# Optimization experiments

Hardware: AMD Instinct MI355X
Metric: run time of the kernel (lower is better)

Reference implementation:

```python
import jax, jax.numpy as jnp
import numpy as np


def _gru_scan(x_seq, Wih, Whh, bih, bhh):
    # x_seq: (S, N, D); PyTorch GRU/GRUCell gate math, h0 = 0. Returns (S, N, H).
    H = Whh.shape[1]
    gi_all = x_seq @ Wih.T + bih  # precompute input projections: (S, N, 3H)

    def step(h, gi):
        gh = h @ Whh.T + bhh
        ir, iz, inn = jnp.split(gi, 3, axis=-1)
        hr, hz, hn = jnp.split(gh, 3, axis=-1)
        r = jax.nn.sigmoid(ir + hr)
        z = jax.nn.sigmoid(iz + hz)
        n = jnp.tanh(inn + r * hn)
        h_new = (1.0 - z) * n + z * h
        return h_new, h_new

    h0 = jnp.zeros((x_seq.shape[1], H), x_seq.dtype)
    _, ys = jax.lax.scan(step, h0, gi_all)
    return ys


def setup_inputs() -> dict:
    key = jax.random.key(0)
    ks = jax.random.split(key, 40)
    B, T = 32, 800
    NOTE, E, P, H0, H1, FE, RE = 128, 256, 256, 512, 512, 64, 64

    def w(k, shape):
        return jax.random.normal(k, shape, dtype=jnp.float32) * 0.05

    return {
        "note": jax.random.randint(ks[0], (B, T), 0, NOTE, dtype=jnp.int64),
        "f0_prev": jax.random.normal(ks[1], (B, T), dtype=jnp.float32),
        "rmse_prev": jax.random.normal(ks[2], (B, T), dtype=jnp.float32),
        "note_emb": w(ks[3], (NOTE, E)),
        "f0_W": w(ks[4], (FE, 1)), "f0_b": w(ks[5], (FE,)),
        "rmse_W": w(ks[6], (RE, 1)), "rmse_b": w(ks[7], (RE,)),
        "pre1_W": w(ks[8], (P, E)), "pre1_b": w(ks[9], (P,)),
        "pre2_W": w(ks[10], (P, P)), "pre2_b": w(ks[11], (P,)),
        "encf_Wih": w(ks[12], (3 * H0, P)), "encf_Whh": w(ks[13], (3 * H0, H0)),
        "encf_bih": w(ks[14], (3 * H0,)), "encf_bhh": w(ks[15], (3 * H0,)),
        "encb_Wih": w(ks[16], (3 * H0, P)), "encb_Whh": w(ks[17], (3 * H0, H0)),
        "encb_bih": w(ks[18], (3 * H0,)), "encb_bhh": w(ks[19], (3 * H0,)),
        "decf_Wih": w(ks[20], (3 * H1, 2 * H0 + FE)), "decf_Whh": w(ks[21], (3 * H1, H1)),
        "decf_bih": w(ks[22], (3 * H1,)), "decf_bhh": w(ks[23], (3 * H1,)),
        "decr_Wih": w(ks[24], (3 * H1, 2 * H0 + RE)), "decr_Whh": w(ks[25], (3 * H1, H1)),
        "decr_bih": w(ks[26], (3 * H1,)), "decr_bhh": w(ks[27], (3 * H1,)),
        "postf_W": w(ks[28], (1, H1)), "postf_b": w(ks[29], (1,)),
        "postr_W": w(ks[30], (1, H1)), "postr_b": w(ks[31], (1,)),
    }


def reference(note, f0_prev, rmse_prev, note_emb, f0_W, f0_b, rmse_W, rmse_b,
              pre1_W, pre1_b, pre2_W, pre2_b,
              encf_Wih, encf_Whh, encf_bih, encf_bhh,
              encb_Wih, encb_Whh, encb_bih, encb_bhh,
              decf_Wih, decf_Whh, decf_bih, decf_bhh,
              decr_Wih, decr_Whh, decr_bih, decr_bhh,
              postf_W, postf_b, postr_W, postr_b):
    # Embeddings. Linear(1, FE) on a [B,T] signal == outer-broadcast with W[:,0].
    ne = note_emb[note]                                   # (B, T, E)
    f0e = f0_prev[..., None] * f0_W[:, 0] + f0_b          # (B, T, FE)
    rme = rmse_prev[..., None] * rmse_W[:, 0] + rmse_b    # (B, T, RE)

    # Prenet: Linear -> Tanh -> Linear -> Tanh
    h = jnp.tanh(jnp.tanh(ne @ pre1_W.T + pre1_b) @ pre2_W.T + pre2_b)  # (B, T, P)

    # Encoder: torch nn.GRU built WITHOUT batch_first and called with lengths=None,
    # so the recurrence runs over axis 0 (B) with T acting as the GRU batch. Replicated.
    ef = _gru_scan(h, encf_Wih, encf_Whh, encf_bih, encf_bhh)            # (B, T, H0)
    eb = _gru_scan(h[::-1], encb_Wih, encb_Whh, encb_bih, encb_bhh)[::-1]
    enc = jnp.concatenate([ef, eb], axis=-1)                             # (B, T, 2H0)

    # Decoders: GRUCell loop over T with teacher forcing (y_prevs has T>1 steps),
    # so step-t input is concat(enc[:, t], embed(prev[:, t])) -> standard scan.
    xt = jnp.transpose(enc, (1, 0, 2))                                   # (T, B, 2H0)
    hf = _gru_scan(jnp.concatenate([xt, jnp.transpose(f0e, (1, 0, 2))], -1),
                   decf_Wih, decf_Whh, decf_bih, decf_bhh)               # (T, B, H1)
    hr = _gru_scan(jnp.concatenate([xt, jnp.transpose(rme, (1, 0, 2))], -1),
                   decr_Wih, decr_Whh, decr_bih, decr_bhh)               # (T, B, H1)

    f0 = jnp.transpose((hf @ postf_W.T + postf_b)[..., 0], (1, 0))       # (B, T)
    rmse = jnp.transpose((hr @ postr_W.T + postr_b)[..., 0], (1, 0))     # (B, T)
    return (f0, rmse)
```

## Files before the change

kernel.cpp:

```cpp
#include <hip/hip_runtime.h>
#include <hip/hip_bf16.h>


typedef __bf16 bf16;
typedef bf16 bf16x8 __attribute__((ext_vector_type(8)));
typedef float f32x4 __attribute__((ext_vector_type(4)));
typedef unsigned int u32x4 __attribute__((ext_vector_type(4)));

#define BATCH 32
#define TLEN 800
#define BT (BATCH * TLEN)

__device__ __forceinline__ float bf2f(bf16 v) {
    unsigned short u = __builtin_bit_cast(unsigned short, v);
    unsigned int x = ((unsigned int)u) << 16;
    return __builtin_bit_cast(float, x);
}
__device__ __forceinline__ bf16 f2bf(float f) {
    unsigned int x = __builtin_bit_cast(unsigned int, f);
    unsigned int r = (x + 0x7FFFu + ((x >> 16) & 1u)) >> 16;
    return __builtin_bit_cast(bf16, (unsigned short)r);
}
__device__ __forceinline__ bf16x8 ld8f(const float* p) {
    f32x4 a = *(const f32x4*)p;
    f32x4 b = *(const f32x4*)(p + 4);
    bf16x8 r;
#pragma unroll
    for (int i = 0; i < 4; i++) {
        r[i] = f2bf(a[i]);
        r[i + 4] = f2bf(b[i]);
    }
    return r;
}
__device__ __forceinline__ void splitv(f32x4 a, f32x4 b, bf16x8& vh, bf16x8& vl) {
#pragma unroll
    for (int j = 0; j < 4; j++) {
        bf16 h0 = f2bf(a[j]);
        vh[j] = h0;
        vl[j] = f2bf(a[j] - bf2f(h0));
        bf16 h1 = f2bf(b[j]);
        vh[j + 4] = h1;
        vl[j + 4] = f2bf(b[j] - bf2f(h1));
    }
}
__device__ __forceinline__ f32x4 mfma16(bf16x8 a, bf16x8 b, f32x4 c) {
    return __builtin_amdgcn_mfma_f32_16x16x32_bf16(a, b, c, 0, 0, 0);
}
__device__ __forceinline__ float sigm(float x) { return 1.f / (1.f + __expf(-x)); }

__device__ __forceinline__ void cst_u32(unsigned int* p, unsigned int v) {
    __hip_atomic_store(p, v, __ATOMIC_RELAXED, __HIP_MEMORY_SCOPE_AGENT);
}
__device__ __forceinline__ unsigned int cld_u32(const unsigned int* p) {
    return __hip_atomic_load(p, __ATOMIC_RELAXED, __HIP_MEMORY_SCOPE_AGENT);
}
__device__ __forceinline__ unsigned long long cld_u64(const unsigned int* p) {
    return __hip_atomic_load((const unsigned long long*)p, __ATOMIC_RELAXED,
                             __HIP_MEMORY_SCOPE_AGENT);
}
__device__ __forceinline__ float pk2f(unsigned int pk) {
    return bf2f(__builtin_bit_cast(bf16, (unsigned short)(pk >> 16))) +
           bf2f(__builtin_bit_cast(bf16, (unsigned short)(pk & 0xFFFFu)));
}
__device__ __forceinline__ void unpk(const unsigned long long q[4], bf16x8& ah,
                                     bf16x8& al) {
    u32x4 hw, lw;
#pragma unroll
    for (int i = 0; i < 4; i++) {
        unsigned int x = (unsigned int)q[i];
        unsigned int y = (unsigned int)(q[i] >> 32);
        hw[i] = __builtin_amdgcn_perm(y, x, 0x07060302u);
        lw[i] = __builtin_amdgcn_perm(y, x, 0x05040100u);
    }
    ah = __builtin_bit_cast(bf16x8, hw);
    al = __builtin_bit_cast(bf16x8, lw);
}

template <int MODE>
__global__ __launch_bounds__(256) void gemm01_k(
    const int* __restrict__ note, const float* __restrict__ asrc,
    const float* __restrict__ W, const float* __restrict__ bias,
    float* __restrict__ out, int t0, int TC) {
    __shared__ bf16 Ah[128][72], Al[128][72], Bs[128][72];

    const int tid = threadIdx.x;
    const int lane = tid & 63, wv = tid >> 6;
    const int wm = wv & 1, wn = wv >> 1;
    const int l15 = lane & 15, hi = lane >> 4;
    const int bm = blockIdx.x * 128, bn = blockIdx.y * 128;
    const int ch = (tid & 7) * 8, arow = tid >> 3;

    f32x4 acc[4][4] = {};
    const float* ap[4];
    if (MODE == 0) {
        int zc = 0;
        for (int i = 0; i < 64; i++) zc += (note[2 * i + 1] == 0) ? 1 : 0;
        const bool n64 = (zc >= 60);
#pragma unroll
        for (int i = 0; i < 4; i++) {
            int m = bm + arow + 32 * i;
            int b = m / TC, tt = m - b * TC;
            int idx = b * TLEN + t0 + tt;
            int id = n64 ? note[2 * idx] : note[idx];
            id = id < 0 ? 0 : (id > 127 ? 127 : id);
            ap[i] = asrc + (size_t)id * 256;
        }
    } else {
#pragma unroll
        for (int i = 0; i < 4; i++) ap[i] = asrc + (size_t)(bm + arow + 32 * i) * 256;
    }

    for (int k0 = 0; k0 < 256; k0 += 64) {
#pragma unroll
        for (int i = 0; i < 4; i++) {
            int row = arow + 32 * i;
            f32x4 va = *(const f32x4*)(ap[i] + k0 + ch);
            f32x4 vb = *(const f32x4*)(ap[i] + k0 + ch + 4);
            bf16x8 vh, vl;
            splitv(va, vb, vh, vl);
            *(bf16x8*)&Ah[row][ch] = vh;
            *(bf16x8*)&Al[row][ch] = vl;
        }
#pragma unroll
        for (int i = 0; i < 4; i++) {
            int row = arow + 32 * i;
            *(bf16x8*)&Bs[row][ch] = ld8f(W + (size_t)(bn + row) * 256 + k0 + ch);
        }
        __syncthreads();
#pragma unroll
        for (int kk = 0; kk < 64; kk += 32) {
            bf16x8 ah[4], al[4], bb[4];
#pragma unroll
            for (int mt = 0; mt < 4; mt++) {
                ah[mt] = *(const bf16x8*)&Ah[wm * 64 + mt * 16 + l15][kk + hi * 8];
                al[mt] = *(const bf16x8*)&Al[wm * 64 + mt * 16 + l15][kk + hi * 8];
            }
#pragma unroll
            for (int nt = 0; nt < 4; nt++)
                bb[nt] = *(const bf16x8*)&Bs[wn * 64 + nt * 16 + l15][kk + hi * 8];
#pragma unroll
            for (int mt = 0; mt < 4; mt++)
#pragma unroll
                for (int nt = 0; nt < 4; nt++) {
                    acc[mt][nt] = mfma16(ah[mt], bb[nt], acc[mt][nt]);
                    acc[mt][nt] = mfma16(al[mt], bb[nt], acc[mt][nt]);
                }
        }
        __syncthreads();
    }

#pragma unroll
    for (int mt = 0; mt < 4; mt++)
#pragma unroll
        for (int nt = 0; nt < 4; nt++) {
            int n = bn + wn * 64 + nt * 16 + l15;
            float bs = bias[n];
#pragma unroll
            for (int r = 0; r < 4; r++) {
                int m = bm + wm * 64 + mt * 16 + hi * 4 + r;
                out[(size_t)m * 256 + n] = tanhf(acc[mt][nt][r] + bs);
            }
        }
}

__global__ __launch_bounds__(256) void gemm2_k(
    const float* __restrict__ ef, const float* __restrict__ eb,
    const float* __restrict__ sig, const float* __restrict__ sigW,
    const float* __restrict__ sigB, const float* __restrict__ W,
    const float* __restrict__ bias, float* __restrict__ out, int t0, int TC) {
    __shared__ bf16 Ah[128][72], Al[128][72];
    __shared__ bf16 Bh[64][72], Bl[64][72];

    const int tid = threadIdx.x;
    const int lane = tid & 63, wv = tid >> 6;
    const int wm = wv & 1, wn = wv >> 1;
    const int l15 = lane & 15, hi = lane >> 4;
    const int bm = blockIdx.x * 128, bn = blockIdx.y * 64;
    const int ch = (tid & 7) * 8, arow = tid >> 3;

    f32x4 acc[4][2] = {};
    int rb[4];
    float sigv[4];
#pragma unroll
    for (int i = 0; i < 4; i++) {
        int m = bm + arow + 32 * i;
        int tt = m >> 5, b = m & 31;
        rb[i] = b * TC + tt;
        sigv[i] = sig[b * TLEN + t0 + tt];
    }

    for (int k0 = 0; k0 < 1088; k0 += 64) {
#pragma unroll
        for (int i = 0; i < 4; i++) {
            int row = arow + 32 * i;
            int k = k0 + ch;
            f32x4 va, vb;
            if (k < 512) {
                va = *(const f32x4*)(ef + (size_t)rb[i] * 512 + k);
                vb = *(const f32x4*)(ef + (size_t)rb[i] * 512 + k + 4);
            } else if (k < 1024) {
                va = *(const f32x4*)(eb + (size_t)rb[i] * 512 + (k - 512));
                vb = *(const f32x4*)(eb + (size_t)rb[i] * 512 + (k - 512) + 4);
            } else {
                f32x4 w0 = *(const f32x4*)(sigW + ch);
                f32x4 w1 = *(const f32x4*)(sigW + ch + 4);
                f32x4 b0 = *(const f32x4*)(sigB + ch);
                f32x4 b1 = *(const f32x4*)(sigB + ch + 4);
                float s = sigv[i];
#pragma unroll
                for (int j = 0; j < 4; j++) {
                    va[j] = s * w0[j] + b0[j];
                    vb[j] = s * w1[j] + b1[j];
                }
            }
            bf16x8 vh, vl;
            splitv(va, vb, vh, vl);
            *(bf16x8*)&Ah[row][ch] = vh;
            *(bf16x8*)&Al[row][ch] = vl;
        }
#pragma unroll
        for (int i = 0; i < 2; i++) {
            int row = arow + 32 * i;
            const float* src = W + (size_t)(bn + row) * 1088 + k0 + ch;
            f32x4 va = *(const f32x4*)src;
            f32x4 vb = *(const f32x4*)(src + 4);
            bf16x8 vh, vl;
            splitv(va, vb, vh, vl);
            *(bf16x8*)&Bh[row][ch] = vh;
            *(bf16x8*)&Bl[row][ch] = vl;
        }
        __syncthreads();
#pragma unroll
        for (int kk = 0; kk < 64; kk += 32) {
            bf16x8 ah[4], al[4], bh[2], bl[2];
#pragma unroll
            for (int mt = 0; mt < 4; mt++) {
                ah[mt] = *(const bf16x8*)&Ah[wm * 64 + mt * 16 + l15][kk + hi * 8];
                al[mt] = *(const bf16x8*)&Al[wm * 64 + mt * 16 + l15][kk + hi * 8];
            }
#pragma unroll
            for (int nt = 0; nt < 2; nt++) {
                bh[nt] = *(const bf16x8*)&Bh[wn * 32 + nt * 16 + l15][kk + hi * 8];
                bl[nt] = *(const bf16x8*)&Bl[wn * 32 + nt * 16 + l15][kk + hi * 8];
            }
#pragma unroll
            for (int mt = 0; mt < 4; mt++)
#pragma unroll
                for (int nt = 0; nt < 2; nt++) {
                    acc[mt][nt] = mfma16(ah[mt], bh[nt], acc[mt][nt]);
                    acc[mt][nt] = mfma16(al[mt], bh[nt], acc[mt][nt]);
                    acc[mt][nt] = mfma16(ah[mt], bl[nt], acc[mt][nt]);
                }
        }
        __syncthreads();
    }

#pragma unroll
    for (int mt = 0; mt < 4; mt++)
#pragma unroll
        for (int nt = 0; nt < 2; nt++) {
            int n = bn + wn * 32 + nt * 16 + l15;
            float bs = bias[n];
#pragma unroll
            for (int r = 0; r < 4; r++) {
                int m = bm + wm * 64 + mt * 16 + hi * 4 + r;
                out[(size_t)m * 1536 + n] = acc[mt][nt][r] + bs;
            }
        }
}

__global__ __launch_bounds__(256) void enc_step_k(
    int step, int TC, const float* __restrict__ hpre, float* __restrict__ efb,
    float* __restrict__ ebb, const float* __restrict__ fWih,
    const float* __restrict__ fWhh, const float* __restrict__ fbih,
    const float* __restrict__ fbhh, const float* __restrict__ bWih,
    const float* __restrict__ bWhh, const float* __restrict__ bbih,
    const float* __restrict__ bbhh) {
    __shared__ bf16 As[32][72], Alo[32][72];
    __shared__ bf16 Bs[96][72], Blo[96][72];

    const int dir = blockIdx.z;
    const float* Wih = dir ? bWih : fWih;
    const float* Whh = dir ? bWhh : fWhh;
    const float* bih = dir ? bbih : fbih;
    const float* bhh = dir ? bbhh : fbhh;
    float* outb = dir ? ebb : efb;
    const int bsrc = dir ? (31 - step) : step;
    const int prevb = dir ? (32 - step) : (step - 1);

    const int tid = threadIdx.x;
    const int lane = tid & 63, wv = tid >> 6;
    const int mt = wv & 1, jt = wv >> 1;
    const int l15 = lane & 15, hi = lane >> 4;
    const int mtile = blockIdx.x, jtile = blockIdx.y;
    const int ch = (tid & 7) * 8, arow = tid >> 3;

    f32x4 acc_r = {}, acc_z = {}, acc_in = {}, acc_hn = {};

    const int nblocks = (step == 0) ? 4 : 12;
    for (int kb = 0; kb < nblocks; kb++) {
        int k0 = kb * 64;
        {
            int trow = mtile * 32 + arow;
            int tcl = trow < TC ? trow : TC - 1;
            const float* src = (k0 < 256)
                                   ? (hpre + ((size_t)bsrc * TC + tcl) * 256 + k0 + ch)
                                   : (outb + ((size_t)prevb * TC + tcl) * 512 + (k0 - 256) + ch);
            f32x4 va = *(const f32x4*)src;
            f32x4 vb = *(const f32x4*)(src + 4);
            bf16x8 vh, vl;
            splitv(va, vb, vh, vl);
            *(bf16x8*)&As[arow][ch] = vh;
            *(bf16x8*)&Alo[arow][ch] = vl;
        }
#pragma unroll
        for (int i = 0; i < 3; i++) {
            int row = arow + 32 * i;
            int s = row >> 5, j = row & 31;
            int wr = s * 512 + jtile * 32 + j;
            const float* src = (k0 < 256) ? (Wih + (size_t)wr * 256 + k0 + ch)
                                          : (Whh + (size_t)wr * 512 + (k0 - 256) + ch);
            f32x4 va = *(const f32x4*)src;
            f32x4 vb = *(const f32x4*)(src + 4);
            bf16x8 vh, vl;
            splitv(va, vb, vh, vl);
            *(bf16x8*)&Bs[row][ch] = vh;
            *(bf16x8*)&Blo[row][ch] = vl;
        }
        __syncthreads();
#pragma unroll
        for (int kk = 0; kk < 64; kk += 32) {
            bf16x8 a = *(const bf16x8*)&As[mt * 16 + l15][kk + hi * 8];
            bf16x8 alo = *(const bf16x8*)&Alo[mt * 16 + l15][kk + hi * 8];
            bf16x8 brh = *(const bf16x8*)&Bs[jt * 16 + l15][kk + hi * 8];
            bf16x8 brl = *(const bf16x8*)&Blo[jt * 16 + l15][kk + hi * 8];
            bf16x8 bzh = *(const bf16x8*)&Bs[32 + jt * 16 + l15][kk + hi * 8];
            bf16x8 bzl = *(const bf16x8*)&Blo[32 + jt * 16 + l15][kk + hi * 8];
            bf16x8 bnh = *(const bf16x8*)&Bs[64 + jt * 16 + l15][kk + hi * 8];
            bf16x8 bnl = *(const bf16x8*)&Blo[64 + jt * 16 + l15][kk + hi * 8];
            acc_r = mfma16(a, brh, acc_r);
            acc_r = mfma16(alo, brh, acc_r);
            acc_r = mfma16(a, brl, acc_r);
            acc_z = mfma16(a, bzh, acc_z);
            acc_z = mfma16(alo, bzh, acc_z);
            acc_z = mfma16(a, bzl, acc_z);
            if (k0 < 256) {
                acc_in = mfma16(a, bnh, acc_in);
                acc_in = mfma16(alo, bnh, acc_in);
                acc_in = mfma16(a, bnl, acc_in);
            } else {
                acc_hn = mfma16(a, bnh, acc_hn);
                acc_hn = mfma16(alo, bnh, acc_hn);
                acc_hn = mfma16(a, bnl, acc_hn);
            }
        }
        __syncthreads();
    }

    int j = jtile * 32 + jt * 16 + l15;
    float bir = bih[j] + bhh[j];
    float biz = bih[512 + j] + bhh[512 + j];
    float bin = bih[1024 + j];
    float bhn = bhh[1024 + j];
#pragma unroll
    for (int r = 0; r < 4; r++) {
        int trow = mtile * 32 + mt * 16 + hi * 4 + r;
        if (trow < TC) {
            float rr = sigm(acc_r[r] + bir);
            float zz = sigm(acc_z[r] + biz);
            float nn = tanhf(acc_in[r] + bin + rr * (acc_hn[r] + bhn));
            float hp = (step > 0) ? outb[((size_t)prevb * TC + trow) * 512 + j] : 0.f;
            outb[((size_t)bsrc * TC + trow) * 512 + j] = (1.f - zz) * nn + zz * hp;
        }
    }
}

__global__ __launch_bounds__(256, 1) void dec_k(
    const float* __restrict__ giF, const float* __restrict__ giR,
    const float* __restrict__ WhhF, const float* __restrict__ WhhR,
    const float* __restrict__ bhhF, const float* __restrict__ bhhR,
    unsigned int* __restrict__ HpkF, unsigned int* __restrict__ HpkR,
    const unsigned int* __restrict__ HpvF, const unsigned int* __restrict__ HpvR,
    int* __restrict__ flags, int t0, int TC) {
    const int d = blockIdx.x >> 4;
    const int g = blockIdx.x & 15;
    const float* gi = d ? giR : giF;
    const float* Whh = d ? WhhR : WhhF;
    const float* bhh = d ? bhhR : bhhF;
    unsigned int* Hpk = d ? HpkR : HpkF;
    const unsigned int* Hpv = d ? HpvR : HpvF;
    int* flg = flags + d * 256;

    const int tid = threadIdx.x;
    const int lane = tid & 63, wv = tid >> 6;
    const int mt = wv & 1, jt = wv >> 1;
    const int l15 = lane & 15, hi = lane >> 4;
    const int j_abs = g * 32 + jt * 16 + l15;
    const int wid = g * 4 + wv;

    bf16x8 Wf[3][16];
#pragma unroll
    for (int s = 0; s < 3; s++)
#pragma unroll
        for (int kb = 0; kb < 16; kb++)
            Wf[s][kb] = ld8f(Whh + (size_t)(s * 512 + j_abs) * 512 + kb * 32 + hi * 8);

    const float bhr = bhh[j_abs];
    const float bhz = bhh[512 + j_abs];
    const float bhn = bhh[1024 + j_abs];

    float hpreg[4] = {0.f, 0.f, 0.f, 0.f};

    for (int tt = 0; tt < TC; tt++) {
        const int t = t0 + tt;
        float gr[4], gz[4], gn[4];
#pragma unroll
        for (int r = 0; r < 4; r++) {
            int b = mt * 16 + hi * 4 + r;
            const float* gp = gi + ((size_t)tt * BATCH + b) * 1536 + j_abs;
            gr[r] = gp[0];
            gz[r] = gp[512];
            gn[r] = gp[1024];
        }

        f32x4 ar = {}, az = {}, an = {};
        float hp[4] = {0.f, 0.f, 0.f, 0.f};
        if (t > 0) {
            const unsigned int* base;
            if (tt > 0) {
                while (true) {
                    int v = __hip_atomic_load(&flg[lane * 4], __ATOMIC_RELAXED,
                                              __HIP_MEMORY_SCOPE_AGENT);
                    if (!__any(v < t)) break;
                    __builtin_amdgcn_s_sleep(1);
                }
                asm volatile("" ::: "memory");
                base = Hpk + (size_t)(tt - 1) * BATCH * 512;
            } else {
                base = Hpv + (size_t)(TC - 1) * BATCH * 512;
            }
            const unsigned int* ap = base + (size_t)(mt * 16 + l15) * 512 + hi * 8;
#pragma unroll
            for (int half = 0; half < 2; half++) {
                unsigned long long q[8][4];
#pragma unroll
                for (int qq = 0; qq < 8; qq++) {
                    const unsigned int* pp = ap + (half * 8 + qq) * 32;
#pragma unroll
                    for (int u = 0; u < 4; u++) q[qq][u] = cld_u64(pp + 2 * u);
                }
#pragma unroll
                for (int qq = 0; qq < 8; qq++) {
                    int kb = half * 8 + qq;
                    bf16x8 ah, al;
                    unpk(q[qq], ah, al);
                    ar = mfma16(ah, Wf[0][kb], ar);
                    ar = mfma16(al, Wf[0][kb], ar);
                    az = mfma16(ah, Wf[1][kb], az);
                    az = mfma16(al, Wf[1][kb], az);
                    an = mfma16(ah, Wf[2][kb], an);
                    an = mfma16(al, Wf[2][kb], an);
                }
            }
            if (tt > 0) {
#pragma unroll
                for (int r = 0; r < 4; r++) hp[r] = hpreg[r];
            } else {
#pragma unroll
                for (int r = 0; r < 4; r++) {
                    int b = mt * 16 + hi * 4 + r;
                    hp[r] = pk2f(cld_u32(base + (size_t)b * 512 + j_abs));
                }
            }
        }
#pragma unroll
        for (int r = 0; r < 4; r++) {
            int b = mt * 16 + hi * 4 + r;
            float rr = sigm(gr[r] + ar[r] + bhr);
            float zz = sigm(gz[r] + az[r] + bhz);
            float nn = tanhf(gn[r] + rr * (an[r] + bhn));
            float hnew = (1.f - zz) * nn + zz * hp[r];
            bf16 hh = f2bf(hnew);
            bf16 hl = f2bf(hnew - bf2f(hh));
            unsigned int pk =
                ((unsigned int)__builtin_bit_cast(unsigned short, hh) << 16) |
                (unsigned int)__builtin_bit_cast(unsigned short, hl);
            cst_u32(&Hpk[((size_t)tt * BATCH + b) * 512 + j_abs], pk);
            hpreg[r] = hnew;
        }
        asm volatile("s_waitcnt vmcnt(0)" ::: "memory");
        if (lane == 0)
            __hip_atomic_store(&flg[wid * 4], t + 1, __ATOMIC_RELAXED,
                               __HIP_MEMORY_SCOPE_AGENT);
    }
}

__global__ __launch_bounds__(256) void post_k(
    const unsigned int* __restrict__ H, const float* __restrict__ W,
    const float* __restrict__ bs, float* __restrict__ out, int t0) {
    const int wv = threadIdx.x >> 6, lane = threadIdx.x & 63;
    const int row = blockIdx.x * 4 + wv;
    const int tt = row >> 5, b = row & 31;
    const float bias = bs[0];
    const unsigned int* hp = H + (size_t)row * 512 + lane * 8;
    u32x4 p0 = *(const u32x4*)hp;
    u32x4 p1 = *(const u32x4*)(hp + 4);
    f32x4 w0 = *(const f32x4*)(W + lane * 8);
    f32x4 w1 = *(const f32x4*)(W + lane * 8 + 4);
    float s = 0.f;
#pragma unroll
    for (int i = 0; i < 4; i++) s += pk2f(p0[i]) * w0[i] + pk2f(p1[i]) * w1[i];
#pragma unroll
    for (int off = 32; off > 0; off >>= 1) s += __shfl_down(s, off);
    if (lane == 0) out[b * TLEN + t0 + tt] = s + bias;
}

__global__ void zero_k(int* __restrict__ flags) {
    int i = blockIdx.x * 256 + threadIdx.x;
    if (i < 2 * TLEN)
        __hip_atomic_store(&flags[i], 0, __ATOMIC_RELAXED,
                           __HIP_MEMORY_SCOPE_AGENT);
}

extern "C" void kernel_launch(void* const* d_in, const int* in_sizes, int n_in,
                              void* d_out, int out_size, void* d_ws, size_t ws_size,
                              hipStream_t stream) {
    const int* note = (const int*)d_in[0];
    const float* f0_prev = (const float*)d_in[1];
    const float* rmse_prev = (const float*)d_in[2];
    const float* note_emb = (const float*)d_in[3];
    const float* f0_W = (const float*)d_in[4];
    const float* f0_b = (const float*)d_in[5];
    const float* rmse_W = (const float*)d_in[6];
    const float* rmse_b = (const float*)d_in[7];
    const float* pre1_W = (const float*)d_in[8];
    const float* pre1_b = (const float*)d_in[9];
    const float* pre2_W = (const float*)d_in[10];
    const float* pre2_b = (const float*)d_in[11];
    const float* encf_Wih = (const float*)d_in[12];
    const float* encf_Whh = (const float*)d_in[13];
    const float* encf_bih = (const float*)d_in[14];
    const float* encf_bhh = (const float*)d_in[15];
    const float* encb_Wih = (const float*)d_in[16];
    const float* encb_Whh = (const float*)d_in[17];
    const float* encb_bih = (const float*)d_in[18];
    const float* encb_bhh = (const float*)d_in[19];
    const float* decf_Wih = (const float*)d_in[20];
    const float* decf_Whh = (const float*)d_in[21];
    const float* decf_bih = (const float*)d_in[22];
    const float* decf_bhh = (const float*)d_in[23];
    const float* decr_Wih = (const float*)d_in[24];
    const float* decr_Whh = (const float*)d_in[25];
    const float* decr_bih = (const float*)d_in[26];
    const float* decr_bhh = (const float*)d_in[27];
    const float* postf_W = (const float*)d_in[28];
    const float* postf_b = (const float*)d_in[29];
    const float* postr_W = (const float*)d_in[30];
    const float* postr_b = (const float*)d_in[31];
    float* out = (float*)d_out;

    const int tcs[9] = {800, 400, 200, 100, 80, 40, 20, 8, 4};
    int TC = 4;
    for (int i = 0; i < 9; i++) {
        int tc = tcs[i];
        int slots = (tc == TLEN) ? 1 : 2;
        size_t need = (size_t)(2 * 65536 + 2 * 196608 + 2 * slots * 65536) * tc + 65536;
        if (ws_size >= need) { TC = tc; break; }
    }
    const int NC = TLEN / TC;
    const int slots = (NC == 1) ? 1 : 2;

    char* ws = (char*)d_ws;
    size_t off = 0;
    auto carve = [&](size_t bytes) {
        void* p = ws + off;
        off += (bytes + 255) & ~(size_t)255;
        return p;
    };
    const size_t slotB = (size_t)65536 * TC;
    float* ef_c = (float*)carve(slotB);
    float* eb_c = (float*)carve(slotB);
    float* giF_c = (float*)carve((size_t)196608 * TC);
    float* giR_c = (float*)carve((size_t)196608 * TC);
    unsigned int* ringF = (unsigned int*)carve(slotB * slots);
    unsigned int* ringR = (unsigned int*)carve(slotB * slots);
    int* flags = (int*)carve(2 * TLEN * 4);
    float* t1_c = giF_c;
    float* hpre_c = giF_c + (size_t)8192 * TC;

    zero_k<<<dim3(7), 256, 0, stream>>>(flags);

    const size_t slotE = (size_t)TC * BATCH * 512;

    for (int c = 0; c < NC; c++) {
        const int t0 = c * TC;
        const int mg = TC * 32 / 128;

        gemm01_k<0><<<dim3(mg, 2), 256, 0, stream>>>(note, note_emb, pre1_W, pre1_b,
                                                     t1_c, t0, TC);
        gemm01_k<1><<<dim3(mg, 2), 256, 0, stream>>>(nullptr, t1_c, pre2_W, pre2_b,
                                                     hpre_c, t0, TC);
        const int etiles = (TC + 31) / 32;
        for (int i = 0; i < 32; i++)
            enc_step_k<<<dim3(etiles, 16, 2), 256, 0, stream>>>(
                i, TC, hpre_c, ef_c, eb_c, encf_Wih, encf_Whh, encf_bih, encf_bhh,
                encb_Wih, encb_Whh, encb_bih, encb_bhh);

        gemm2_k<<<dim3(mg, 24), 256, 0, stream>>>(ef_c, eb_c, f0_prev, f0_W, f0_b,
                                                  decf_Wih, decf_bih, giF_c, t0, TC);
        gemm2_k<<<dim3(mg, 24), 256, 0, stream>>>(ef_c, eb_c, rmse_prev, rmse_W,
                                                  rmse_b, decr_Wih, decr_bih, giR_c,
                                                  t0, TC);

        unsigned int* HcurF = ringF + (size_t)(c & (slots - 1)) * slotE;
        const unsigned int* HprevF = ringF + (size_t)((c - 1) & (slots - 1)) * slotE;
        unsigned int* HcurR = ringR + (size_t)(c & (slots - 1)) * slotE;
        const unsigned int* HprevR = ringR + (size_t)((c - 1) & (slots - 1)) * slotE;

        dec_k<<<dim3(32), 256, 0, stream>>>(giF_c, giR_c, decf_Whh, decr_Whh,
                                            decf_bhh, decr_bhh, HcurF, HcurR,
                                            HprevF, HprevR, flags, t0, TC);

        post_k<<<dim3(TC * 32 / 4), 256, 0, stream>>>(HcurF, postf_W, postf_b,
                                                      out, t0);
        post_k<<<dim3(TC * 32 / 4), 256, 0, stream>>>(HcurR, postr_W, postr_b,
                                                      out + BT, t0);
    }
    (void)in_sizes; (void)n_in; (void)out_size; (void)ws_size;
}
```

Measured before the change: 12.61 ms.

## Hoist encoder input projection into batched GEMM and widen decoder blocks

The encoder input projection (hpre @ Wih) now runs as one batched GEMM per direction (a new MODE 2 of gemm01_k) before the 32 sequential encoder steps. Each step then loads the precomputed gates and only does the recurrent Whh matmul, which removes redundant K work from the serial chain. The persistent decoder kernel now runs 16 blocks of 512 threads instead of 32 of 256, so there are fewer flags to poll and one block-level barrier before each flag store. Scratch buffers are reassigned to the ring slots. This adds memory traffic for the precomputed gates and a __syncthreads per decoder timestep.

```diff
diff --git a/kernel.cpp b/kernel.cpp
--- a/kernel.cpp
+++ b/kernel.cpp
@@ -89,6 +89,7 @@
     const int l15 = lane & 15, hi = lane >> 4;
     const int bm = blockIdx.x * 128, bn = blockIdx.y * 128;
     const int ch = (tid & 7) * 8, arow = tid >> 3;
+    const int LDC = (MODE == 2) ? 1536 : 256;
 
     f32x4 acc[4][4] = {};
     const float* ap[4];
@@ -154,11 +155,12 @@
 #pragma unroll
         for (int nt = 0; nt < 4; nt++) {
             int n = bn + wn * 64 + nt * 16 + l15;
-            float bs = bias[n];
+            float bs = (MODE == 2) ? 0.f : bias[n];
 #pragma unroll
             for (int r = 0; r < 4; r++) {
                 int m = bm + wm * 64 + mt * 16 + hi * 4 + r;
-                out[(size_t)m * 256 + n] = tanhf(acc[mt][nt][r] + bs);
+                float v = acc[mt][nt][r] + bs;
+                out[(size_t)m * LDC + n] = (MODE == 2) ? v : tanhf(v);
             }
         }
 }
@@ -270,17 +272,17 @@
 }
 
 __global__ __launch_bounds__(256) void enc_step_k(
-    int step, int TC, const float* __restrict__ hpre, float* __restrict__ efb,
-    float* __restrict__ ebb, const float* __restrict__ fWih,
-    const float* __restrict__ fWhh, const float* __restrict__ fbih,
-    const float* __restrict__ fbhh, const float* __restrict__ bWih,
+    int step, int TC, const float* __restrict__ egiF,
+    const float* __restrict__ egiB, float* __restrict__ efb,
+    float* __restrict__ ebb, const float* __restrict__ fWhh,
+    const float* __restrict__ fbih, const float* __restrict__ fbhh,
     const float* __restrict__ bWhh, const float* __restrict__ bbih,
     const float* __restrict__ bbhh) {
     __shared__ bf16 As[32][72], Alo[32][72];
     __shared__ bf16 Bs[96][72], Blo[96][72];
 
     const int dir = blockIdx.z;
-    const float* Wih = dir ? bWih : fWih;
+    const float* egi = dir ? egiB : egiF;
     const float* Whh = dir ? bWhh : fWhh;
     const float* bih = dir ? bbih : fbih;
     const float* bhh = dir ? bbhh : fbhh;
@@ -294,70 +296,72 @@
     const int l15 = lane & 15, hi = lane >> 4;
     const int mtile = blockIdx.x, jtile = blockIdx.y;
     const int ch = (tid & 7) * 8, arow = tid >> 3;
-
-    f32x4 acc_r = {}, acc_z = {}, acc_in = {}, acc_hn = {};
-
-    const int nblocks = (step == 0) ? 4 : 12;
-    for (int kb = 0; kb < nblocks; kb++) {
-        int k0 = kb * 64;
-        {
-            int trow = mtile * 32 + arow;
-            int tcl = trow < TC ? trow : TC - 1;
-            const float* src = (k0 < 256)
-                                   ? (hpre + ((size_t)bsrc * TC + tcl) * 256 + k0 + ch)
-                                   : (outb + ((size_t)prevb * TC + tcl) * 512 + (k0 - 256) + ch);
-            f32x4 va = *(const f32x4*)src;
-            f32x4 vb = *(const f32x4*)(src + 4);
-            bf16x8 vh, vl;
-            splitv(va, vb, vh, vl);
-            *(bf16x8*)&As[arow][ch] = vh;
-            *(bf16x8*)&Alo[arow][ch] = vl;
-        }
-#pragma unroll
-        for (int i = 0; i < 3; i++) {
-            int row = arow + 32 * i;
-            int s = row >> 5, j = row & 31;
-            int wr = s * 512 + jtile * 32 + j;
-            const float* src = (k0 < 256) ? (Wih + (size_t)wr * 256 + k0 + ch)
-                                          : (Whh + (size_t)wr * 512 + (k0 - 256) + ch);
-            f32x4 va = *(const f32x4*)src;
-            f32x4 vb = *(const f32x4*)(src + 4);
-            bf16x8 vh, vl;
-            splitv(va, vb, vh, vl);
-            *(bf16x8*)&Bs[row][ch] = vh;
-            *(bf16x8*)&Blo[row][ch] = vl;
-        }
-        __syncthreads();
-#pragma unroll
-        for (int kk = 0; kk < 64; kk += 32) {
-            bf16x8 a = *(const bf16x8*)&As[mt * 16 + l15][kk + hi * 8];
-            bf16x8 alo = *(const bf16x8*)&Alo[mt * 16 + l15][kk + hi * 8];
-            bf16x8 brh = *(const bf16x8*)&Bs[jt * 16 + l15][kk + hi * 8];
-            bf16x8 brl = *(const bf16x8*)&Blo[jt * 16 + l15][kk + hi * 8];
-            bf16x8 bzh = *(const bf16x8*)&Bs[32 + jt * 16 + l15][kk + hi * 8];
-            bf16x8 bzl = *(const bf16x8*)&Blo[32 + jt * 16 + l15][kk + hi * 8];
-            bf16x8 bnh = *(const bf16x8*)&Bs[64 + jt * 16 + l15][kk + hi * 8];
-            bf16x8 bnl = *(const bf16x8*)&Blo[64 + jt * 16 + l15][kk + hi * 8];
-            acc_r = mfma16(a, brh, acc_r);
-            acc_r = mfma16(alo, brh, acc_r);
-            acc_r = mfma16(a, brl, acc_r);
-            acc_z = mfma16(a, bzh, acc_z);
-            acc_z = mfma16(alo, bzh, acc_z);
-            acc_z = mfma16(a, bzl, acc_z);
-            if (k0 < 256) {
-                acc_in = mfma16(a, bnh, acc_in);
-                acc_in = mfma16(alo, bnh, acc_in);
-                acc_in = mfma16(a, bnl, acc_in);
-            } else {
+    const int j = jtile * 32 + jt * 16 + l15;
+
+    f32x4 acc_r, acc_z, acc_in;
+    f32x4 acc_hn = {};
+#pragma unroll
+    for (int r = 0; r < 4; r++) {
+        int trow = mtile * 32 + mt * 16 + hi * 4 + r;
+        int tcl = trow < TC ? trow : TC - 1;
+        const float* ep = egi + ((size_t)bsrc * TC + tcl) * 1536 + j;
+        acc_r[r] = ep[0];
+        acc_z[r] = ep[512];
+        acc_in[r] = ep[1024];
+    }
+
+    if (step > 0) {
+        for (int kb = 0; kb < 8; kb++) {
+            int k0 = kb * 64;
+            {
+                int trow = mtile * 32 + arow;
+                int tcl = trow < TC ? trow : TC - 1;
+                const float* src = outb + ((size_t)prevb * TC + tcl) * 512 + k0 + ch;
+                f32x4 va = *(const f32x4*)src;
+                f32x4 vb = *(const f32x4*)(src + 4);
+                bf16x8 vh, vl;
+                splitv(va, vb, vh, vl);
+                *(bf16x8*)&As[arow][ch] = vh;
+                *(bf16x8*)&Alo[arow][ch] = vl;
+            }
+#pragma unroll
+            for (int i = 0; i < 3; i++) {
+                int row = arow + 32 * i;
+                int s = row >> 5, jj = row & 31;
+                const float* src =
+                    Whh + (size_t)(s * 512 + jtile * 32 + jj) * 512 + k0 + ch;
+                f32x4 va = *(const f32x4*)src;
+                f32x4 vb = *(const f32x4*)(src + 4);
+                bf16x8 vh, vl;
+                splitv(va, vb, vh, vl);
+                *(bf16x8*)&Bs[row][ch] = vh;
+                *(bf16x8*)&Blo[row][ch] = vl;
+            }
+            __syncthreads();
+#pragma unroll
+            for (int kk = 0; kk < 64; kk += 32) {
+                bf16x8 a = *(const bf16x8*)&As[mt * 16 + l15][kk + hi * 8];
+                bf16x8 alo = *(const bf16x8*)&Alo[mt * 16 + l15][kk + hi * 8];
+                bf16x8 brh = *(const bf16x8*)&Bs[jt * 16 + l15][kk + hi * 8];
+                bf16x8 brl = *(const bf16x8*)&Blo[jt * 16 + l15][kk + hi * 8];
+                bf16x8 bzh = *(const bf16x8*)&Bs[32 + jt * 16 + l15][kk + hi * 8];
+                bf16x8 bzl = *(const bf16x8*)&Blo[32 + jt * 16 + l15][kk + hi * 8];
+                bf16x8 bnh = *(const bf16x8*)&Bs[64 + jt * 16 + l15][kk + hi * 8];
+                bf16x8 bnl = *(const bf16x8*)&Blo[64 + jt * 16 + l15][kk + hi * 8];
+                acc_r = mfma16(a, brh, acc_r);
+                acc_r = mfma16(alo, brh, acc_r);
+                acc_r = mfma16(a, brl, acc_r);
+                acc_z = mfma16(a, bzh, acc_z);
+                acc_z = mfma16(alo, bzh, acc_z);
+                acc_z = mfma16(a, bzl, acc_z);
                 acc_hn = mfma16(a, bnh, acc_hn);
                 acc_hn = mfma16(alo, bnh, acc_hn);
                 acc_hn = mfma16(a, bnl, acc_hn);
             }
-        }
-        __syncthreads();
-    }
-
-    int j = jtile * 32 + jt * 16 + l15;
+            __syncthreads();
+        }
+    }
+
     float bir = bih[j] + bhh[j];
     float biz = bih[512 + j] + bhh[512 + j];
     float bin = bih[1024 + j];
@@ -375,28 +379,27 @@
     }
 }
 
-__global__ __launch_bounds__(256, 1) void dec_k(
+__global__ __launch_bounds__(512, 1) void dec_k(
     const float* __restrict__ giF, const float* __restrict__ giR,
     const float* __restrict__ WhhF, const float* __restrict__ WhhR,
     const float* __restrict__ bhhF, const float* __restrict__ bhhR,
     unsigned int* __restrict__ HpkF, unsigned int* __restrict__ HpkR,
     const unsigned int* __restrict__ HpvF, const unsigned int* __restrict__ HpvR,
     int* __restrict__ flags, int t0, int TC) {
-    const int d = blockIdx.x >> 4;
-    const int g = blockIdx.x & 15;
+    const int d = blockIdx.x >> 3;
+    const int g = blockIdx.x & 7;
     const float* gi = d ? giR : giF;
     const float* Whh = d ? WhhR : WhhF;
     const float* bhh = d ? bhhR : bhhF;
     unsigned int* Hpk = d ? HpkR : HpkF;
     const unsigned int* Hpv = d ? HpvR : HpvF;
-    int* flg = flags + d * 256;
+    int* flg = flags + d * 64;
 
     const int tid = threadIdx.x;
     const int lane = tid & 63, wv = tid >> 6;
     const int mt = wv & 1, jt = wv >> 1;
     const int l15 = lane & 15, hi = lane >> 4;
-    const int j_abs = g * 32 + jt * 16 + l15;
-    const int wid = g * 4 + wv;
+    const int j_abs = g * 64 + jt * 16 + l15;
 
     bf16x8 Wf[3][16];
 #pragma unroll
@@ -429,7 +432,7 @@
             const unsigned int* base;
             if (tt > 0) {
                 while (true) {
-                    int v = __hip_atomic_load(&flg[lane * 4], __ATOMIC_RELAXED,
+                    int v = __hip_atomic_load(&flg[(lane & 7) * 4], __ATOMIC_RELAXED,
                                               __HIP_MEMORY_SCOPE_AGENT);
                     if (!__any(v < t)) break;
                     __builtin_amdgcn_s_sleep(1);
@@ -489,8 +492,9 @@
             hpreg[r] = hnew;
         }
         asm volatile("s_waitcnt vmcnt(0)" ::: "memory");
-        if (lane == 0)
-            __hip_atomic_store(&flg[wid * 4], t + 1, __ATOMIC_RELAXED,
+        __syncthreads();
+        if (tid == 0)
+            __hip_atomic_store(&flg[g * 4], t + 1, __ATOMIC_RELAXED,
                                __HIP_MEMORY_SCOPE_AGENT);
     }
 }
@@ -585,8 +589,9 @@
     unsigned int* ringF = (unsigned int*)carve(slotB * slots);
     unsigned int* ringR = (unsigned int*)carve(slotB * slots);
     int* flags = (int*)carve(2 * TLEN * 4);
-    float* t1_c = giF_c;
-    float* hpre_c = giF_c + (size_t)8192 * TC;
+
+    float* egiF = giF_c;
+    float* egiB = giR_c;
 
     zero_k<<<dim3(7), 256, 0, stream>>>(flags);
 
@@ -595,16 +600,25 @@
     for (int c = 0; c < NC; c++) {
         const int t0 = c * TC;
         const int mg = TC * 32 / 128;
+        const int cs = c & (slots - 1), ps = (c - 1) & (slots - 1);
+
+        float* t1_c = (float*)(ringF + (size_t)cs * slotE);
+        float* hpre_c = (float*)(ringR + (size_t)cs * slotE);
 
         gemm01_k<0><<<dim3(mg, 2), 256, 0, stream>>>(note, note_emb, pre1_W, pre1_b,
                                                      t1_c, t0, TC);
         gemm01_k<1><<<dim3(mg, 2), 256, 0, stream>>>(nullptr, t1_c, pre2_W, pre2_b,
                                                      hpre_c, t0, TC);
+        gemm01_k<2><<<dim3(mg, 12), 256, 0, stream>>>(nullptr, hpre_c, encf_Wih,
+                                                      nullptr, egiF, t0, TC);
+        gemm01_k<2><<<dim3(mg, 12), 256, 0, stream>>>(nullptr, hpre_c, encb_Wih,
+                                                      nullptr, egiB, t0, TC);
+
         const int etiles = (TC + 31) / 32;
         for (int i = 0; i < 32; i++)
             enc_step_k<<<dim3(etiles, 16, 2), 256, 0, stream>>>(
-                i, TC, hpre_c, ef_c, eb_c, encf_Wih, encf_Whh, encf_bih, encf_bhh,
-                encb_Wih, encb_Whh, encb_bih, encb_bhh);
+                i, TC, egiF, egiB, ef_c, eb_c, encf_Whh, encf_bih, encf_bhh,
+                encb_Whh, encb_bih, encb_bhh);
 
         gemm2_k<<<dim3(mg, 24), 256, 0, stream>>>(ef_c, eb_c, f0_prev, f0_W, f0_b,
                                                   decf_Wih, decf_bih, giF_c, t0, TC);
@@ -612,12 +626,12 @@
                                                   rmse_b, decr_Wih, decr_bih, giR_c,
                                                   t0, TC);
 
-        unsigned int* HcurF = ringF + (size_t)(c & (slots - 1)) * slotE;
-        const unsigned int* HprevF = ringF + (size_t)((c - 1) & (slots - 1)) * slotE;
-        unsigned int* HcurR = ringR + (size_t)(c & (slots - 1)) * slotE;
-        const unsigned int* HprevR = ringR + (size_t)((c - 1) & (slots - 1)) * slotE;
-
-        dec_k<<<dim3(32), 256, 0, stream>>>(giF_c, giR_c, decf_Whh, decr_Whh,
+        unsigned int* HcurF = ringF + (size_t)cs * slotE;
+        const unsigned int* HprevF = ringF + (size_t)ps * slotE;
+        unsigned int* HcurR = ringR + (size_t)cs * slotE;
+        const unsigned int* HprevR = ringR + (size_t)ps * slotE;
+
+        dec_k<<<dim3(16), 512, 0, stream>>>(giF_c, giR_c, decf_Whh, decr_Whh,
                                             decf_bhh, decr_bhh, HcurF, HcurR,
                                             HprevF, HprevR, flags, t0, TC);
 
```

Result: slower. 19.00 ms (+50.7%).
